# Optimization experiments

Measured on AMD Instinct MI355X. Metric: run time of the kernel, lower is better.

## Reference

```python
import jax, jax.numpy as jnp
import numpy as np

N_HEADS = 16
D_EMBED = 1024
SEQ = 1024  # must equal D_EMBED: GroupNorm is applied on dim1 of (b, seq, c)
BATCH = 4
GROUPS = 32
EPS = 1e-6


def setup_inputs() -> dict:
    key = jax.random.key(0)
    ks = jax.random.split(key, 7)
    c = D_EMBED
    s = 0.02
    return {
        "x": jax.random.normal(ks[0], (BATCH, SEQ, c), dtype=jnp.float32),
        "gn_w": jnp.ones((SEQ,), dtype=jnp.float32),  # GroupNorm affine over dim1 (= seq here)
        "gn_b": jnp.zeros((SEQ,), dtype=jnp.float32),
        "w_qkv": jax.random.normal(ks[1], (3 * c, c), dtype=jnp.float32) * s,
        "b_qkv": jnp.zeros((3 * c,), dtype=jnp.float32),
        "w_out": jax.random.normal(ks[2], (c, c), dtype=jnp.float32) * s,
        "b_out": jnp.zeros((c,), dtype=jnp.float32),
    }


def _group_norm_dim1(x, w, b):
    # Faithful to torch.nn.GroupNorm applied to (B, S, C): dim1 (S) is the
    # channel dim; normalize over each group of S//GROUPS rows together with C.
    bsz, s, c = x.shape
    xg = x.reshape(bsz, GROUPS, (s // GROUPS) * c)
    mu = jnp.mean(xg, axis=-1, keepdims=True)
    var = jnp.var(xg, axis=-1, keepdims=True)
    xn = ((xg - mu) * jax.lax.rsqrt(var + EPS)).reshape(bsz, s, c)
    return xn * w[None, :, None] + b[None, :, None]


def reference(x, gn_w, gn_b, w_qkv, b_qkv, w_out, b_out):
    bsz, seq, c = x.shape
    dh = c // N_HEADS
    h = _group_norm_dim1(x, gn_w, gn_b)
    qkv = h @ w_qkv.T + b_qkv  # (b, s, 3c)
    q, k, v = jnp.split(qkv, 3, axis=-1)
    # (b, s, H, dh) -> (b, H, s, dh)
    q = q.reshape(bsz, seq, N_HEADS, dh).transpose(0, 2, 1, 3)
    k = k.reshape(bsz, seq, N_HEADS, dh).transpose(0, 2, 1, 3)
    v = v.reshape(bsz, seq, N_HEADS, dh).transpose(0, 2, 1, 3)
    # NOTE: source divides by sqrt(d_head) TWICE -> effective scale 1/d_head
    w = jnp.einsum("bhqd,bhkd->bhqk", q, k) / float(dh)
    w = jax.nn.softmax(w, axis=-1)
    o = jnp.einsum("bhqk,bhkd->bhqd", w, v)  # (b, H, s, dh)
    # NOTE: source calls .transpose(1,2) without assignment, then .view(b,s,c):
    # faithful behavior is a raw reshape of the (b, H, s, dh) tensor.
    o = o.reshape(bsz, seq, c)
    o = o @ w_out.T + b_out
    return x + o
```

## Files before the change

kernel.cpp:

```cpp
#include <hip/hip_runtime.h>

typedef __bf16 bf16_t;
typedef bf16_t bf16x8 __attribute__((ext_vector_type(8)));
typedef bf16_t bf16x4 __attribute__((ext_vector_type(4)));
typedef float f32x4 __attribute__((ext_vector_type(4)));

__device__ __forceinline__ void gload_lds16(const bf16_t* g, bf16_t* l) {
    __builtin_amdgcn_global_load_lds(
        (const __attribute__((address_space(1))) void*)g,
        (__attribute__((address_space(3))) void*)l, 16, 0, 0);
}

__global__ __launch_bounds__(256) void cvt_bf16_kernel(const float* __restrict__ in1,
                                                       const float* __restrict__ in2,
                                                       bf16_t* __restrict__ out1,
                                                       bf16_t* __restrict__ out2,
                                                       int n1_4, int ntot_4) {
    int i = blockIdx.x * 256 + threadIdx.x;
    if (i >= ntot_4) return;
    const float* in = (i < n1_4) ? in1 : in2;
    bf16_t* out = (i < n1_4) ? out1 : out2;
    int j = (i < n1_4) ? i : i - n1_4;
    float4 v = reinterpret_cast<const float4*>(in)[j];
    bf16x4 o;
    o[0] = (bf16_t)v.x; o[1] = (bf16_t)v.y; o[2] = (bf16_t)v.z; o[3] = (bf16_t)v.w;
    *reinterpret_cast<bf16x4*>(out + (size_t)j * 4) = o;
}

__global__ __launch_bounds__(256, 2) void groupnorm_kernel(const float* __restrict__ x,
        const float* __restrict__ gw, const float* __restrict__ gb,
        bf16_t* __restrict__ h) {
    int bg = blockIdx.x;
    int batch = bg >> 5, g = bg & 31;
    const float* xp = x + ((size_t)batch * 1024 + g * 32) * 1024;
    float4 xr[32];
    float s = 0.f, s2 = 0.f;
    #pragma unroll
    for (int i = 0; i < 32; ++i) {
        float4 v = reinterpret_cast<const float4*>(xp)[threadIdx.x + i * 256];
        xr[i] = v;
        s  += v.x + v.y + v.z + v.w;
        s2 += v.x*v.x + v.y*v.y + v.z*v.z + v.w*v.w;
    }
    #pragma unroll
    for (int o = 32; o >= 1; o >>= 1) {
        s  += __shfl_down(s, o, 64);
        s2 += __shfl_down(s2, o, 64);
    }
    __shared__ float ps[4], ps2[4];
    __shared__ float stat[2];
    if ((threadIdx.x & 63) == 0) { ps[threadIdx.x >> 6] = s; ps2[threadIdx.x >> 6] = s2; }
    __syncthreads();
    if (threadIdx.x == 0) {
        float S  = ps[0] + ps[1] + ps[2] + ps[3];
        float S2 = ps2[0] + ps2[1] + ps2[2] + ps2[3];
        float mu  = S * (1.f / 32768.f);
        float var = S2 * (1.f / 32768.f) - mu * mu;
        stat[0] = mu; stat[1] = rsqrtf(var + 1e-6f);
    }
    __syncthreads();
    float mu = stat[0], rs = stat[1];
    bf16_t* hp = h + ((size_t)batch * 1024 + g * 32) * 1024;
    #pragma unroll
    for (int i = 0; i < 32; ++i) {
        int idx = threadIdx.x + i * 256;
        int row = idx >> 8;
        float a = rs * gw[g * 32 + row];
        float b = gb[g * 32 + row] - mu * a;
        float4 v = xr[i];
        bf16x4 o;
        o[0] = (bf16_t)(v.x * a + b); o[1] = (bf16_t)(v.y * a + b);
        o[2] = (bf16_t)(v.z * a + b); o[3] = (bf16_t)(v.w * a + b);
        *reinterpret_cast<bf16x4*>(hp + (size_t)idx * 4) = o;
    }
}

__global__ __launch_bounds__(512, 2) void gemm256_kernel(
        const bf16_t* __restrict__ A, const bf16_t* __restrict__ W,
        const float* __restrict__ bias, bf16_t* __restrict__ outp,
        int M, int N, int K) {
    __shared__ bf16_t As[2][2][128 * 64];
    __shared__ bf16_t Bs[2][2][128 * 64];
    int nbx = N >> 8;
    int cpx = gridDim.x >> 3;
    int bid = blockIdx.x;
    int tile = (bid & 7) * cpx + (bid >> 3);
    int bx = tile % nbx, by = tile / nbx;
    int m0 = by * 256, n0 = bx * 256;
    int t = threadIdx.x, l = t & 63, wid = t >> 6;
    int lr = l & 15, lg = l >> 4;
    int wm = (wid >> 2) * 128, wn = (wid & 3) * 64;
    int ah = wid >> 2;
    int bh = (wid & 3) >> 1;
    int bnl = wn & 64;

    int c0 = t, c1 = t + 512;
    int r0 = c0 >> 3, col0 = (((c0 & 7) ^ (r0 & 7)) << 3);
    int r1 = c1 >> 3, col1 = (((c1 & 7) ^ (r1 & 7)) << 3);

    f32x4 acc[8][4] = {};

#define STAGE_A(slot, hf, kt) { \
        const bf16_t* _s = A + (size_t)(m0 + (hf) * 128) * K + (kt) * 64; \
        gload_lds16(_s + (size_t)r0 * K + col0, &As[slot][hf][c0 * 8]); \
        gload_lds16(_s + (size_t)r1 * K + col1, &As[slot][hf][c1 * 8]); }
#define STAGE_B(slot, hf, kt) { \
        const bf16_t* _s = W + (size_t)(n0 + (hf) * 128) * K + (kt) * 64; \
        gload_lds16(_s + (size_t)r0 * K + col0, &Bs[slot][hf][c0 * 8]); \
        gload_lds16(_s + (size_t)r1 * K + col1, &Bs[slot][hf][c1 * 8]); }
#define LOAD_AF(mh) \
        _Pragma("unroll") \
        for (int i = 0; i < 4; ++i) { \
            int row = (mh) * 64 + i * 16 + lr; \
            _Pragma("unroll") \
            for (int kk = 0; kk < 2; ++kk) \
                afr[i][kk] = *reinterpret_cast<const bf16x8*>( \
                    &As[cur][ah][row * 64 + (((kk * 4 + lg) ^ (row & 7)) << 3)]); }
#define LOAD_BF(dst, nh) \
        _Pragma("unroll") \
        for (int j = 0; j < 2; ++j) { \
            int col = bnl + (nh) * 32 + j * 16 + lr; \
            _Pragma("unroll") \
            for (int kk = 0; kk < 2; ++kk) \
                dst[j][kk] = *reinterpret_cast<const bf16x8*>( \
                    &Bs[cur][bh][col * 64 + (((kk * 4 + lg) ^ (col & 7)) << 3)]); }
#define MFMA_Q(mh, nh, bfr) \
        __builtin_amdgcn_s_setprio(1); \
        _Pragma("unroll") \
        for (int i = 0; i < 4; ++i) \
            _Pragma("unroll") \
            for (int j = 0; j < 2; ++j) \
                _Pragma("unroll") \
                for (int kk = 0; kk < 2; ++kk) \
                    acc[(mh) * 4 + i][(nh) * 2 + j] = __builtin_amdgcn_mfma_f32_16x16x32_bf16( \
                        afr[i][kk], bfr[j][kk], acc[(mh) * 4 + i][(nh) * 2 + j], 0, 0, 0); \
        __builtin_amdgcn_s_setprio(0);

    STAGE_A(0, 0, 0) STAGE_B(0, 0, 0) STAGE_B(0, 1, 0) STAGE_A(0, 1, 0)
    asm volatile("s_waitcnt vmcnt(0)" ::: "memory");
    __builtin_amdgcn_s_barrier();

    const int NT = K >> 6;
    for (int kt = 0; kt < NT - 1; ++kt) {
        int cur = kt & 1, nxt = cur ^ 1;
        bf16x8 afr[4][2], bf0[2][2], bf1[2][2];
        LOAD_AF(0) LOAD_BF(bf0, 0)
        STAGE_A(nxt, 0, kt + 1)
        __builtin_amdgcn_s_barrier();
        MFMA_Q(0, 0, bf0)
        asm volatile("s_waitcnt vmcnt(4)" ::: "memory");
        __builtin_amdgcn_s_barrier();
        LOAD_BF(bf1, 1)
        STAGE_B(nxt, 0, kt + 1)
        __builtin_amdgcn_s_barrier();
        MFMA_Q(0, 1, bf1)
        asm volatile("s_waitcnt vmcnt(4)" ::: "memory");
        __builtin_amdgcn_s_barrier();
        LOAD_AF(1)
        STAGE_B(nxt, 1, kt + 1)
        __builtin_amdgcn_s_barrier();
        MFMA_Q(1, 1, bf1)
        __builtin_amdgcn_s_barrier();
        STAGE_A(nxt, 1, kt + 1)
        __builtin_amdgcn_s_barrier();
        MFMA_Q(1, 0, bf0)
        asm volatile("s_waitcnt vmcnt(4)" ::: "memory");
        __builtin_amdgcn_s_barrier();
    }
    {
        int cur = (NT - 1) & 1;
        asm volatile("s_waitcnt vmcnt(0)" ::: "memory");
        __builtin_amdgcn_s_barrier();
        bf16x8 afr[4][2], bf0[2][2], bf1[2][2];
        LOAD_AF(0) LOAD_BF(bf0, 0) LOAD_BF(bf1, 1)
        MFMA_Q(0, 0, bf0)
        MFMA_Q(0, 1, bf1)
        LOAD_AF(1)
        MFMA_Q(1, 1, bf1)
        MFMA_Q(1, 0, bf0)
    }

    #pragma unroll
    for (int mf = 0; mf < 8; ++mf) {
        #pragma unroll
        for (int r = 0; r < 4; ++r) {
            int row = m0 + wm + mf * 16 + lg * 4 + r;
            #pragma unroll
            for (int nf = 0; nf < 4; ++nf) {
                int col = n0 + wn + nf * 16 + lr;
                outp[(size_t)row * N + col] = (bf16_t)(acc[mf][nf][r] + bias[col]);
            }
        }
    }
#undef STAGE_A
#undef STAGE_B
#undef LOAD_AF
#undef LOAD_BF
#undef MFMA_Q
}

template <int EPI, int BM>
__global__ __launch_bounds__(256) void gemm_nt_kernel(
        const bf16_t* __restrict__ A, const bf16_t* __restrict__ W,
        const float* __restrict__ bias, void* __restrict__ outp,
        const float* __restrict__ resid, int M, int N, int K, int lda) {
    constexpr int MF = BM / 32;
    __shared__ bf16_t As[BM * 64];
    __shared__ bf16_t Bs[128 * 64];
    int nbx = N >> 7;
    int cpx = gridDim.x >> 3;
    int bid = blockIdx.x;
    int tile = (bid & 7) * cpx + (bid >> 3);
    int bx = tile % nbx, by = tile / nbx;
    int m0 = by * BM, n0 = bx * 128;
    int t = threadIdx.x, l = t & 63, wid = t >> 6;
    int wm = (wid >> 1) * (BM / 2), wn = (wid & 1) * 64;
    int lr = l & 15, lg = l >> 4;

    f32x4 acc[MF][4] = {};
    for (int k0 = 0; k0 < K; k0 += 64) {
        #pragma unroll
        for (int i = 0; i < BM / 32; ++i) {
            int c = t + i * 256;
            int row = c >> 3, cc = c & 7;
            int col = (cc ^ (row & 7)) << 3;
            gload_lds16(A + (size_t)(m0 + row) * lda + k0 + col, &As[c * 8]);
        }
        #pragma unroll
        for (int i = 0; i < 4; ++i) {
            int c = t + i * 256;
            int row = c >> 3, cc = c & 7;
            int col = (cc ^ (row & 7)) << 3;
            gload_lds16(W + (size_t)(n0 + row) * K + k0 + col, &Bs[c * 8]);
        }
        __syncthreads();
        #pragma unroll
        for (int s = 0; s < 2; ++s) {
            int xo = ((s * 4 + lg) ^ (lr & 7)) << 3;
            bf16x8 af[MF], bfr[4];
            #pragma unroll
            for (int mf = 0; mf < MF; ++mf)
                af[mf] = *reinterpret_cast<const bf16x8*>(&As[(wm + mf * 16 + lr) * 64 + xo]);
            #pragma unroll
            for (int nf = 0; nf < 4; ++nf)
                bfr[nf] = *reinterpret_cast<const bf16x8*>(&Bs[(wn + nf * 16 + lr) * 64 + xo]);
            #pragma unroll
            for (int mf = 0; mf < MF; ++mf) {
                #pragma unroll
                for (int nf = 0; nf < 4; ++nf)
                    acc[mf][nf] = __builtin_amdgcn_mfma_f32_16x16x32_bf16(af[mf], bfr[nf], acc[mf][nf], 0, 0, 0);
            }
        }
        __syncthreads();
    }
    #pragma unroll
    for (int mf = 0; mf < MF; ++mf) {
        #pragma unroll
        for (int r = 0; r < 4; ++r) {
            int row = m0 + wm + mf * 16 + lg * 4 + r;
            #pragma unroll
            for (int nf = 0; nf < 4; ++nf) {
                int col = n0 + wn + nf * 16 + lr;
                float v = acc[mf][nf][r] + bias[col];
                if (EPI == 0) {
                    reinterpret_cast<bf16_t*>(outp)[(size_t)row * N + col] = (bf16_t)v;
                } else {
                    size_t idx = (size_t)row * N + col;
                    reinterpret_cast<float*>(outp)[idx] = v + resid[idx];
                }
            }
        }
    }
}

__global__ __launch_bounds__(256) void frag_prep_kernel(const bf16_t* __restrict__ qkv,
                                                        bf16_t* __restrict__ kfrag,
                                                        bf16_t* __restrict__ vfrag) {
    __shared__ bf16_t vt[32 * 72];
    int t = threadIdx.x;
    int kt = blockIdx.x & 31, bh = blockIdx.x >> 5;
    int b = bh >> 4, hh = bh & 15;
    const bf16_t* kbase = qkv + ((size_t)b * 1024 + kt * 32) * 3072 + 1024 + hh * 64;
    const bf16_t* vbase = kbase + 1024;
    {
        int row = t >> 3, c = t & 7;
        bf16x8 v = *reinterpret_cast<const bf16x8*>(vbase + (size_t)row * 3072 + c * 8);
        *reinterpret_cast<bf16x8*>(&vt[row * 72 + c * 8]) = v;
    }
    {
        int f = (t >> 7) & 1, m = (t >> 6) & 1, l = t & 63;
        bf16x8 v = *reinterpret_cast<const bf16x8*>(
            kbase + (size_t)(f * 16 + (l & 15)) * 3072 + m * 32 + ((l >> 4) & 3) * 8);
        *reinterpret_cast<bf16x8*>(kfrag + ((size_t)bh * 32 + kt) * 2048 + t * 8) = v;
    }
    __syncthreads();
    {
        int nf = (t >> 6) & 3, l = t & 63;
        int d = nf * 16 + (l & 15);
        int lg = (l >> 4) & 3;
        bf16x8 o;
        #pragma unroll
        for (int j = 0; j < 8; ++j) {
            int kpos = lg * 8 + j;
            int kl = ((kpos & 4) << 2) | ((kpos & 24) >> 1) | (kpos & 3);
            o[j] = vt[kl * 72 + d];
        }
        *reinterpret_cast<bf16x8*>(vfrag + ((size_t)bh * 32 + kt) * 2048 + t * 8) = o;
    }
}

__global__ __launch_bounds__(256, 2) void attn_kernel(const bf16_t* __restrict__ qkv,
                                                      const bf16_t* __restrict__ kfrag,
                                                      const bf16_t* __restrict__ vfrag,
                                                      bf16_t* __restrict__ oq) {
    int bid = blockIdx.x;
    int tile = (bid & 7) * 64 + (bid >> 3);
    int qt = tile & 7, bh = tile >> 3;
    int hh = bh & 15, bb = bh >> 4;
    int t = threadIdx.x, l = t & 63, wid = t >> 6;
    int lr = l & 15, lg = (l >> 4) & 3;

    bf16x8 qf[2][2];
    #pragma unroll
    for (int s = 0; s < 2; ++s) {
        int qrow = qt * 128 + wid * 32 + s * 16 + lr;
        const bf16_t* qp = qkv + ((size_t)bb * 1024 + qrow) * 3072 + hh * 64;
        bf16x8 q0 = *reinterpret_cast<const bf16x8*>(qp + lg * 8);
        bf16x8 q1 = *reinterpret_cast<const bf16x8*>(qp + 32 + lg * 8);
        #pragma unroll
        for (int j = 0; j < 8; ++j) {
            qf[s][0][j] = (bf16_t)((float)q0[j] * 0.02254211001f);
            qf[s][1][j] = (bf16_t)((float)q1[j] * 0.02254211001f);
        }
    }

    const bf16_t* kfb = kfrag + (size_t)bh * 65536 + l * 8;
    const bf16_t* vfb = vfrag + (size_t)bh * 65536 + l * 8;

    f32x4 acc[2][4] = {};
    float den0 = 0.f, den1 = 0.f;

    bf16x8 kA[4], vA[4], kB[4], vB[4];

#define LOADSET(kS, vS, tt) { \
        const bf16_t* _k = kfb + (tt) * 2048; \
        const bf16_t* _v = vfb + (tt) * 2048; \
        kS[0] = *reinterpret_cast<const bf16x8*>(_k); \
        kS[1] = *reinterpret_cast<const bf16x8*>(_k + 512); \
        kS[2] = *reinterpret_cast<const bf16x8*>(_k + 1024); \
        kS[3] = *reinterpret_cast<const bf16x8*>(_k + 1536); \
        vS[0] = *reinterpret_cast<const bf16x8*>(_v); \
        vS[1] = *reinterpret_cast<const bf16x8*>(_v + 512); \
        vS[2] = *reinterpret_cast<const bf16x8*>(_v + 1024); \
        vS[3] = *reinterpret_cast<const bf16x8*>(_v + 1536); }

#define EX(x) __builtin_amdgcn_exp2f(x)

#define COMPUTE(kS, vS) { \
        f32x4 z00 = {0.f,0.f,0.f,0.f}, z01 = {0.f,0.f,0.f,0.f}; \
        f32x4 z10 = {0.f,0.f,0.f,0.f}, z11 = {0.f,0.f,0.f,0.f}; \
        z00 = __builtin_amdgcn_mfma_f32_16x16x32_bf16(kS[0], qf[0][0], z00, 0, 0, 0); \
        z10 = __builtin_amdgcn_mfma_f32_16x16x32_bf16(kS[0], qf[1][0], z10, 0, 0, 0); \
        z01 = __builtin_amdgcn_mfma_f32_16x16x32_bf16(kS[2], qf[0][0], z01, 0, 0, 0); \
        z11 = __builtin_amdgcn_mfma_f32_16x16x32_bf16(kS[2], qf[1][0], z11, 0, 0, 0); \
        z00 = __builtin_amdgcn_mfma_f32_16x16x32_bf16(kS[1], qf[0][1], z00, 0, 0, 0); \
        z10 = __builtin_amdgcn_mfma_f32_16x16x32_bf16(kS[1], qf[1][1], z10, 0, 0, 0); \
        z01 = __builtin_amdgcn_mfma_f32_16x16x32_bf16(kS[3], qf[0][1], z01, 0, 0, 0); \
        z11 = __builtin_amdgcn_mfma_f32_16x16x32_bf16(kS[3], qf[1][1], z11, 0, 0, 0); \
        float a0 = EX(z00[0]), a1 = EX(z00[1]), a2 = EX(z00[2]), a3 = EX(z00[3]); \
        float a4 = EX(z01[0]), a5 = EX(z01[1]), a6 = EX(z01[2]), a7 = EX(z01[3]); \
        float b0 = EX(z10[0]), b1 = EX(z10[1]), b2 = EX(z10[2]), b3 = EX(z10[3]); \
        float b4 = EX(z11[0]), b5 = EX(z11[1]), b6 = EX(z11[2]), b7 = EX(z11[3]); \
        den0 += ((a0 + a1) + (a2 + a3)) + ((a4 + a5) + (a6 + a7)); \
        den1 += ((b0 + b1) + (b2 + b3)) + ((b4 + b5) + (b6 + b7)); \
        bf16x8 pa0, pa1; \
        pa0[0] = (bf16_t)a0; pa0[1] = (bf16_t)a1; pa0[2] = (bf16_t)a2; pa0[3] = (bf16_t)a3; \
        pa0[4] = (bf16_t)a4; pa0[5] = (bf16_t)a5; pa0[6] = (bf16_t)a6; pa0[7] = (bf16_t)a7; \
        pa1[0] = (bf16_t)b0; pa1[1] = (bf16_t)b1; pa1[2] = (bf16_t)b2; pa1[3] = (bf16_t)b3; \
        pa1[4] = (bf16_t)b4; pa1[5] = (bf16_t)b5; pa1[6] = (bf16_t)b6; pa1[7] = (bf16_t)b7; \
        acc[0][0] = __builtin_amdgcn_mfma_f32_16x16x32_bf16(pa0, vS[0], acc[0][0], 0, 0, 0); \
        acc[0][1] = __builtin_amdgcn_mfma_f32_16x16x32_bf16(pa0, vS[1], acc[0][1], 0, 0, 0); \
        acc[0][2] = __builtin_amdgcn_mfma_f32_16x16x32_bf16(pa0, vS[2], acc[0][2], 0, 0, 0); \
        acc[0][3] = __builtin_amdgcn_mfma_f32_16x16x32_bf16(pa0, vS[3], acc[0][3], 0, 0, 0); \
        acc[1][0] = __builtin_amdgcn_mfma_f32_16x16x32_bf16(pa1, vS[0], acc[1][0], 0, 0, 0); \
        acc[1][1] = __builtin_amdgcn_mfma_f32_16x16x32_bf16(pa1, vS[1], acc[1][1], 0, 0, 0); \
        acc[1][2] = __builtin_amdgcn_mfma_f32_16x16x32_bf16(pa1, vS[2], acc[1][2], 0, 0, 0); \
        acc[1][3] = __builtin_amdgcn_mfma_f32_16x16x32_bf16(pa1, vS[3], acc[1][3], 0, 0, 0); }

    LOADSET(kA, vA, 0)
    for (int kt = 0; kt < 32; kt += 2) {
        __builtin_amdgcn_s_barrier();
        LOADSET(kB, vB, kt + 1)
        COMPUTE(kA, vA)
        if (kt + 2 < 32) LOADSET(kA, vA, kt + 2)
        COMPUTE(kB, vB)
    }
#undef LOADSET
#undef COMPUTE
#undef EX

    float rs0[4], rs1[4];
    {
        float v0 = den0, v1 = den1;
        v0 += __shfl_xor(v0, 16, 64);
        v0 += __shfl_xor(v0, 32, 64);
        v1 += __shfl_xor(v1, 16, 64);
        v1 += __shfl_xor(v1, 32, 64);
        #pragma unroll
        for (int r = 0; r < 4; ++r) {
            rs0[r] = 1.f / __shfl(v0, (l & 48) | (lg * 4 + r), 64);
            rs1[r] = 1.f / __shfl(v1, (l & 48) | (lg * 4 + r), 64);
        }
    }

    size_t obase = ((size_t)bh * 1024 + qt * 128 + wid * 32) * 64;
    #pragma unroll
    for (int s = 0; s < 2; ++s) {
        #pragma unroll
        for (int nf = 0; nf < 4; ++nf) {
            #pragma unroll
            for (int r = 0; r < 4; ++r) {
                int q = s * 16 + lg * 4 + r;
                int d = nf * 16 + lr;
                size_t flat = obase + (size_t)q * 64 + d;
                float dn = s == 0 ? rs0[r] : rs1[r];
                oq[(flat >> 10) * 3072 + 1024 + (flat & 1023)] =
                    (bf16_t)(acc[s][nf][r] * dn);
            }
        }
    }
}

extern "C" void kernel_launch(void* const* d_in, const int* in_sizes, int n_in,
                              void* d_out, int out_size, void* d_ws, size_t ws_size,
                              hipStream_t stream) {
    const float* x     = (const float*)d_in[0];
    const float* gn_w  = (const float*)d_in[1];
    const float* gn_b  = (const float*)d_in[2];
    const float* w_qkv = (const float*)d_in[3];
    const float* b_qkv = (const float*)d_in[4];
    const float* w_out = (const float*)d_in[5];
    const float* b_out = (const float*)d_in[6];
    float* out = (float*)d_out;

    bf16_t* h      = (bf16_t*)d_ws;
    bf16_t* wqkv_b = h + (size_t)4096 * 1024;
    bf16_t* wout_b = wqkv_b + (size_t)3072 * 1024;
    bf16_t* qkvb   = wout_b + (size_t)1024 * 1024;
    bf16_t* kfrag  = qkvb + (size_t)4096 * 3072;
    bf16_t* vfrag  = h;

    const int n1_4 = 3072 * 1024 / 4, ntot_4 = n1_4 + 1024 * 1024 / 4;
    cvt_bf16_kernel<<<(ntot_4 + 255) / 256, 256, 0, stream>>>(w_qkv, w_out, wqkv_b, wout_b, n1_4, ntot_4);
    groupnorm_kernel<<<128, 256, 0, stream>>>(x, gn_w, gn_b, h);
    gemm256_kernel<<<192, 512, 0, stream>>>(h, wqkv_b, b_qkv, qkvb, 4096, 3072, 1024);
    frag_prep_kernel<<<2048, 256, 0, stream>>>(qkvb, kfrag, vfrag);
    attn_kernel<<<512, 256, 0, stream>>>(qkvb, kfrag, vfrag, qkvb);
    gemm_nt_kernel<1, 64><<<512, 256, 0, stream>>>(qkvb + 1024, wout_b, b_out, (void*)out, x,
                                                   4096, 1024, 1024, 3072);
}
```

Baseline: 97.95 us.

## Restructure QKV GEMM prefetch schedule to stage A two tiles ahead

Reworks the 256x256 QKV GEMM main loop so half of the next-next A tile is prefetched into the slot just consumed, letting global loads run further ahead. It also removes the peeled final iteration, using wraparound tile indices and looser vmcnt waits. The output projection GEMM is separately switched to a 128-wide tile config with half the blocks. The wraparound loads do redundant work on the last iterations, and the reuse of the current slot relies on precise barrier ordering, so a mistake there would be a race.

```diff
diff --git a/kernel.cpp b/kernel.cpp
--- a/kernel.cpp
+++ b/kernel.cpp
@@ -108,23 +108,23 @@
         const bf16_t* _s = W + (size_t)(n0 + (hf) * 128) * K + (kt) * 64; \
         gload_lds16(_s + (size_t)r0 * K + col0, &Bs[slot][hf][c0 * 8]); \
         gload_lds16(_s + (size_t)r1 * K + col1, &Bs[slot][hf][c1 * 8]); }
-#define LOAD_AF(mh) \
+#define LOAD_AF(slot, mq) \
         _Pragma("unroll") \
         for (int i = 0; i < 4; ++i) { \
-            int row = (mh) * 64 + i * 16 + lr; \
+            int row = (mq) * 64 + i * 16 + lr; \
             _Pragma("unroll") \
             for (int kk = 0; kk < 2; ++kk) \
                 afr[i][kk] = *reinterpret_cast<const bf16x8*>( \
-                    &As[cur][ah][row * 64 + (((kk * 4 + lg) ^ (row & 7)) << 3)]); }
-#define LOAD_BF(dst, nh) \
+                    &As[slot][ah][row * 64 + (((kk * 4 + lg) ^ (row & 7)) << 3)]); }
+#define LOAD_BF(slot, dst, nq) \
         _Pragma("unroll") \
         for (int j = 0; j < 2; ++j) { \
-            int col = bnl + (nh) * 32 + j * 16 + lr; \
+            int col = bnl + (nq) * 32 + j * 16 + lr; \
             _Pragma("unroll") \
             for (int kk = 0; kk < 2; ++kk) \
                 dst[j][kk] = *reinterpret_cast<const bf16x8*>( \
-                    &Bs[cur][bh][col * 64 + (((kk * 4 + lg) ^ (col & 7)) << 3)]); }
-#define MFMA_Q(mh, nh, bfr) \
+                    &Bs[slot][bh][col * 64 + (((kk * 4 + lg) ^ (col & 7)) << 3)]); }
+#define MFMA_Q(mq, nq, bfr) \
         __builtin_amdgcn_s_setprio(1); \
         _Pragma("unroll") \
         for (int i = 0; i < 4; ++i) \
@@ -132,52 +132,42 @@
             for (int j = 0; j < 2; ++j) \
                 _Pragma("unroll") \
                 for (int kk = 0; kk < 2; ++kk) \
-                    acc[(mh) * 4 + i][(nh) * 2 + j] = __builtin_amdgcn_mfma_f32_16x16x32_bf16( \
-                        afr[i][kk], bfr[j][kk], acc[(mh) * 4 + i][(nh) * 2 + j], 0, 0, 0); \
+                    acc[(mq) * 4 + i][(nq) * 2 + j] = __builtin_amdgcn_mfma_f32_16x16x32_bf16( \
+                        afr[i][kk], bfr[j][kk], acc[(mq) * 4 + i][(nq) * 2 + j], 0, 0, 0); \
         __builtin_amdgcn_s_setprio(0);
 
+    const int NT = K >> 6;
+
     STAGE_A(0, 0, 0) STAGE_B(0, 0, 0) STAGE_B(0, 1, 0) STAGE_A(0, 1, 0)
-    asm volatile("s_waitcnt vmcnt(0)" ::: "memory");
+    STAGE_A(1, 0, 1)
+    asm volatile("s_waitcnt vmcnt(2)" ::: "memory");
     __builtin_amdgcn_s_barrier();
 
-    const int NT = K >> 6;
-    for (int kt = 0; kt < NT - 1; ++kt) {
-        int cur = kt & 1, nxt = cur ^ 1;
+    for (int kt = 0; kt < NT; ++kt) {
+        int s = kt & 1, sn = s ^ 1;
+        int k1 = (kt + 1) % NT, k2 = (kt + 2) % NT;
         bf16x8 afr[4][2], bf0[2][2], bf1[2][2];
-        LOAD_AF(0) LOAD_BF(bf0, 0)
-        STAGE_A(nxt, 0, kt + 1)
+        LOAD_AF(s, 0) LOAD_BF(s, bf0, 0)
+        STAGE_B(sn, 0, k1)
+        STAGE_A(sn, 1, k1)
         __builtin_amdgcn_s_barrier();
         MFMA_Q(0, 0, bf0)
-        asm volatile("s_waitcnt vmcnt(4)" ::: "memory");
-        __builtin_amdgcn_s_barrier();
-        LOAD_BF(bf1, 1)
-        STAGE_B(nxt, 0, kt + 1)
+        __builtin_amdgcn_s_barrier();
+        LOAD_BF(s, bf1, 1)
+        STAGE_B(sn, 1, k1)
         __builtin_amdgcn_s_barrier();
         MFMA_Q(0, 1, bf1)
-        asm volatile("s_waitcnt vmcnt(4)" ::: "memory");
-        __builtin_amdgcn_s_barrier();
-        LOAD_AF(1)
-        STAGE_B(nxt, 1, kt + 1)
+        __builtin_amdgcn_s_barrier();
+        LOAD_AF(s, 1)
         __builtin_amdgcn_s_barrier();
         MFMA_Q(1, 1, bf1)
         __builtin_amdgcn_s_barrier();
-        STAGE_A(nxt, 1, kt + 1)
+        LOAD_BF(s, bf0, 0)
+        STAGE_A(s, 0, k2)
         __builtin_amdgcn_s_barrier();
         MFMA_Q(1, 0, bf0)
-        asm volatile("s_waitcnt vmcnt(4)" ::: "memory");
-        __builtin_amdgcn_s_barrier();
-    }
-    {
-        int cur = (NT - 1) & 1;
-        asm volatile("s_waitcnt vmcnt(0)" ::: "memory");
-        __builtin_amdgcn_s_barrier();
-        bf16x8 afr[4][2], bf0[2][2], bf1[2][2];
-        LOAD_AF(0) LOAD_BF(bf0, 0) LOAD_BF(bf1, 1)
-        MFMA_Q(0, 0, bf0)
-        MFMA_Q(0, 1, bf1)
-        LOAD_AF(1)
-        MFMA_Q(1, 1, bf1)
-        MFMA_Q(1, 0, bf0)
+        asm volatile("s_waitcnt vmcnt(2)" ::: "memory");
+        __builtin_amdgcn_s_barrier();
     }
 
     #pragma unroll
@@ -456,6 +446,6 @@
     gemm256_kernel<<<192, 512, 0, stream>>>(h, wqkv_b, b_qkv, qkvb, 4096, 3072, 1024);
     frag_prep_kernel<<<2048, 256, 0, stream>>>(qkvb, kfrag, vfrag);
     attn_kernel<<<512, 256, 0, stream>>>(qkvb, kfrag, vfrag, qkvb);
-    gemm_nt_kernel<1, 64><<<512, 256, 0, stream>>>(qkvb + 1024, wout_b, b_out, (void*)out, x,
-                                                   4096, 1024, 1024, 3072);
-}
+    gemm_nt_kernel<1, 128><<<256, 256, 0, stream>>>(qkvb + 1024, wout_b, b_out, (void*)out, x,
+                                                    4096, 1024, 1024, 3072);
+}
```

Measured after the change: 106.0 us. +8.2%, slower.
